# Kernel optimization log

Hardware: AMD Instinct MI355X
Metric: run time of the kernel (lower is better)

The kernel has to match this reference:

```python
import jax, jax.numpy as jnp
import numpy as np

N_NODES = 100000
N_REL = 6
E_PER_REL = 100000
HID = 256
EMB = 256
N_GRAPHS = 128
N_NODE_TYPES = 4
SUBTYPE_BUCKETS = 256


def setup_inputs() -> dict:
    key = jax.random.key(0)
    ks = jax.random.split(key, 20)
    s = 0.05
    return {
        "x_type": jax.random.randint(ks[0], (N_NODES,), 0, N_NODE_TYPES),
        "x_sub": jax.random.randint(ks[1], (N_NODES,), 0, SUBTYPE_BUCKETS),
        "edges": jax.random.randint(ks[2], (N_REL, 2, E_PER_REL), 0, N_NODES),
        "batch_ids": jnp.sort(jax.random.randint(ks[3], (N_NODES,), 0, N_GRAPHS)),
        "n_graphs": N_GRAPHS,
        "type_emb": jax.random.normal(ks[4], (N_NODE_TYPES, HID // 2), jnp.float32) * s,
        "sub_emb": jax.random.normal(ks[5], (SUBTYPE_BUCKETS, HID // 2), jnp.float32) * s,
        "W_rel0": jax.random.normal(ks[6], (N_REL, HID, HID), jnp.float32) * s,
        "W_self0": jax.random.normal(ks[7], (HID, HID), jnp.float32) * s,
        "b0": jnp.zeros((HID,), jnp.float32),
        "W_rel1": jax.random.normal(ks[8], (N_REL, HID, HID), jnp.float32) * s,
        "W_self1": jax.random.normal(ks[9], (HID, HID), jnp.float32) * s,
        "b1": jnp.zeros((HID,), jnp.float32),
        "pW1": jax.random.normal(ks[10], (HID, HID), jnp.float32) * s,
        "pb1": jnp.zeros((HID,), jnp.float32),
        "pW2": jax.random.normal(ks[11], (HID, EMB), jnp.float32) * s,
        "pb2": jnp.zeros((EMB,), jnp.float32),
    }


def _rgcn_layer(h, edges, W_rel, W_self, b, n):
    # edges: (R, 2, E); h: (N, H)
    src, tgt = edges[:, 0, :], edges[:, 1, :]  # (R, E)
    # per-relation gather -> matmul: (R, E, H) @ (R, H, D) -> (R, E, D)
    msg = jnp.einsum('reh,rhd->red', h[src], W_rel)
    tgt_flat = tgt.reshape(-1)
    out = jax.ops.segment_sum(msg.reshape(-1, msg.shape[-1]), tgt_flat, num_segments=n)
    total_deg = jax.ops.segment_sum(jnp.ones_like(tgt_flat, dtype=h.dtype), tgt_flat, num_segments=n)
    total_deg = jnp.clip(total_deg, 1.0)[:, None]
    out = out / total_deg + h @ W_self + b
    return jax.nn.relu(out)


def _mean_pool(h, batch_ids, n_graphs):
    summed = jax.ops.segment_sum(h, batch_ids, num_segments=n_graphs)
    count = jax.ops.segment_sum(jnp.ones((h.shape[0],), h.dtype), batch_ids, num_segments=n_graphs)
    return summed / jnp.clip(count, 1.0)[:, None]


def reference(x_type, x_sub, edges, batch_ids, n_graphs, type_emb, sub_emb,
              W_rel0, W_self0, b0, W_rel1, W_self1, b1, pW1, pb1, pW2, pb2):
    n = x_type.shape[0]
    h = jnp.concatenate([type_emb[x_type], sub_emb[x_sub]], axis=-1)  # (N, HID)
    h = _rgcn_layer(h, edges, W_rel0, W_self0, b0, n)
    h = _rgcn_layer(h, edges, W_rel1, W_self1, b1, n)
    pooled = _mean_pool(h, batch_ids, n_graphs)  # (G, HID)
    return jax.nn.relu(pooled @ pW1 + pb1) @ pW2 + pb2  # (G, EMB)
```

## Files before the change

### kernel.cpp

```cpp
#include <hip/hip_runtime.h>

#define NN    100000
#define NEDGE 100000
#define NRELS 6
#define HIDD  256
#define NGR   128
#define NKEY  (NRELS * NN)
#define NEDGT (NRELS * NEDGE)
#define WFRAG_ELEMS (4 * 7 * 16 * 2 * 64 * 8)
#define SMASK 0xFFFFF

typedef __bf16 bf16;
typedef __bf16 bf16x4 __attribute__((ext_vector_type(4)));
typedef __bf16 bf16x8 __attribute__((ext_vector_type(8)));
typedef float  f32x4  __attribute__((ext_vector_type(4)));
typedef float  f32x16 __attribute__((ext_vector_type(16)));

__device__ __forceinline__ float readlane_f(float v, int sl) {
    return __int_as_float(__builtin_amdgcn_readlane(__float_as_int(v), sl));
}

__global__ __launch_bounds__(256)
void hist_kernel(const int* __restrict__ edges, int* __restrict__ hist)
{
    int i = blockIdx.x * 256 + threadIdx.x;
    if (i >= NEDGT) return;
    int r = i / NEDGE;
    int e = i - r * NEDGE;
    int t = edges[r * (2 * NEDGE) + NEDGE + e];
    atomicAdd(&hist[r * NN + t], 1);
}

__global__ __launch_bounds__(256)
void scan_l0(const int* __restrict__ in, int* __restrict__ out, int* __restrict__ bsum, int n)
{
    __shared__ int sdata[256];
    const int t = threadIdx.x;
    const int base = blockIdx.x * 2048 + t * 8;
    int v[8]; int s = 0;
#pragma unroll
    for (int i = 0; i < 8; ++i) {
        int idx = base + i;
        int x = (idx < n) ? in[idx] : 0;
        v[i] = s; s += x;
    }
    sdata[t] = s;
    __syncthreads();
    for (int off = 1; off < 256; off <<= 1) {
        int y = (t >= off) ? sdata[t - off] : 0;
        __syncthreads();
        sdata[t] += y;
        __syncthreads();
    }
    int excl = sdata[t] - s;
#pragma unroll
    for (int i = 0; i < 8; ++i) {
        int idx = base + i;
        if (idx < n) out[idx] = excl + v[i];
    }
    if (t == 0) bsum[blockIdx.x] = sdata[255];
}

__global__ __launch_bounds__(256)
void scan_l1(int* __restrict__ bsum, int n)
{
    __shared__ int sdata[256];
    const int t = threadIdx.x;
    const int base = t * 8;
    int v[8]; int s = 0;
#pragma unroll
    for (int i = 0; i < 8; ++i) {
        int idx = base + i;
        int x = (idx < n) ? bsum[idx] : 0;
        v[i] = s; s += x;
    }
    sdata[t] = s;
    __syncthreads();
    for (int off = 1; off < 256; off <<= 1) {
        int y = (t >= off) ? sdata[t - off] : 0;
        __syncthreads();
        sdata[t] += y;
        __syncthreads();
    }
    int excl = sdata[t] - s;
#pragma unroll
    for (int i = 0; i < 8; ++i) {
        int idx = base + i;
        if (idx < n) bsum[idx] = excl + v[i];
    }
}

__global__ __launch_bounds__(256)
void scan_l2(int* __restrict__ offs, int* __restrict__ cursor, const int* __restrict__ bsum,
             const int* __restrict__ hist, float* __restrict__ invdeg,
             const int* __restrict__ batch_ids, float* __restrict__ cnt, int n)
{
    int idx = blockIdx.x * 256 + threadIdx.x;
    if (idx == 0) offs[NKEY] = NEDGT;

    {
        const int lane = threadIdx.x & 63;
        const bool valid = idx < NN;
        const int gv = valid ? batch_ids[idx] : -1;
        const int gprev = __shfl(gv, lane - 1);
        const bool head = valid && (lane == 0 || gv != gprev);
        const bool stop = head || !valid;
        const unsigned long long mask = __ballot(stop);
        if (head) {
            unsigned long long above = (lane == 63) ? 0ull : (mask >> (lane + 1));
            const int next = above ? (lane + 1 + __builtin_ctzll(above)) : 64;
            atomicAdd(&cnt[gv], (float)(next - lane));
        }
    }

    if (idx < NN) {
        int d = 0;
#pragma unroll
        for (int r = 0; r < NRELS; ++r) d += hist[r * NN + idx];
        invdeg[idx] = 1.0f / fmaxf((float)d, 1.0f);
    }
    if (idx >= n) return;
    int v = offs[idx] + bsum[idx >> 11];
    offs[idx] = v;
    cursor[idx] = v;
}

__global__ __launch_bounds__(256)
void scatter_kernel(const int* __restrict__ edges, int* __restrict__ cursor,
                    int* __restrict__ epack)
{
    int i = blockIdx.x * 256 + threadIdx.x;
    if (i >= NEDGT) return;
    int r = i / NEDGE;
    int e = i - r * NEDGE;
    int s = edges[r * (2 * NEDGE) + e];
    int t = edges[r * (2 * NEDGE) + NEDGE + e];
    int pos = atomicAdd(&cursor[r * NN + t], 1);
    epack[pos] = s | ((t & 15) << 20);
}

__global__ __launch_bounds__(256)
void build_wfrag(const float* __restrict__ Wr0, const float* __restrict__ Ws0,
                 const float* __restrict__ Wr1, const float* __restrict__ Ws1,
                 bf16* __restrict__ Wf0, bf16* __restrict__ Wf1)
{
    const int seg = blockIdx.x;
    const int step = blockIdx.y;
    const int layer = blockIdx.z;
    const int tid = threadIdx.x;
    const int w = tid >> 6;
    const int lane = tid & 63;
    const int l31 = lane & 31;
    const int lhi = lane >> 5;

    const float* Wr = layer ? Wr1 : Wr0;
    const float* Ws = layer ? Ws1 : Ws0;
    const float* src = (seg < 6) ? (Wr + ((size_t)seg << 16)) : Ws;
    bf16* Wf = layer ? Wf1 : Wf0;

    const int kb = step * 16 + lhi * 8;
#pragma unroll
    for (int ct = 0; ct < 2; ++ct) {
        const int n = w * 64 + ct * 32 + l31;
        bf16x8 o;
#pragma unroll
        for (int j = 0; j < 8; ++j)
            o[j] = (bf16)src[(size_t)(kb + j) * 256 + n];
        const size_t fb_idx = (size_t)(((w * 7 + seg) * 16 + step) * 2 + ct) * 64 + lane;
        *(bf16x8*)(Wf + fb_idx * 8) = o;
    }
}

template<bool L0, bool POOL>
__global__ __launch_bounds__(256, 3)
void rgcn_fused(const bf16* __restrict__ hin,
                const int* __restrict__ xt, const int* __restrict__ xs,
                const float* __restrict__ temb, const float* __restrict__ semb,
                const bf16* __restrict__ Wfrag, const float* __restrict__ bias,
                const float* __restrict__ invdeg, const int* __restrict__ offs,
                const int* __restrict__ epack, const int* __restrict__ batch_ids,
                float* __restrict__ pooled, bf16* __restrict__ hout)
{
    constexpr int DEPTH = L0 ? 8 : 16;
    const int m0 = blockIdx.x * 64;
    const int tid = threadIdx.x;
    const int lane = tid & 63;
    const int w = tid >> 6;
    const int l31 = lane & 31;
    const int lhi = lane >> 5;
    const int rbase = w * 16;

    __shared__ __align__(16) bf16 As[64 * HIDD];

    f32x16 acc[2][2] = {};

    int ivrow = m0 + rbase + (lane & 15);
    if (ivrow >= NN) ivrow = NN - 1;
    const float ivreg = invdeg[ivrow];

    for (int seg = 0; seg < 7; ++seg) {
        __syncthreads();

#pragma unroll
        for (int z = 0; z < 8; ++z) {
            const int row = rbase + lhi * 8 + z;
            const int unit = row * 32 + (l31 ^ (row & 7));
            *(bf16x8*)&As[unit * 8] = (bf16x8)(bf16)0.0f;
        }

        if (seg == 6) {
#pragma unroll
            for (int z = 0; z < 8; ++z) {
                const int row = rbase + lhi * 8 + z;
                const int gr = m0 + row;
                if (gr < NN) {
                    bf16x8 o;
                    if (L0) {
                        const int f0 = l31 * 8;
                        const float* src = (f0 < 128) ? (temb + xt[gr] * 128 + f0)
                                                      : (semb + xs[gr] * 128 + (f0 - 128));
                        f32x4 x0 = *(const f32x4*)src;
                        f32x4 x1 = *(const f32x4*)(src + 4);
                        o[0] = (bf16)x0[0]; o[1] = (bf16)x0[1];
                        o[2] = (bf16)x0[2]; o[3] = (bf16)x0[3];
                        o[4] = (bf16)x1[0]; o[5] = (bf16)x1[1];
                        o[6] = (bf16)x1[2]; o[7] = (bf16)x1[3];
                    } else {
                        o = *(const bf16x8*)(hin + ((size_t)gr << 8) + l31 * 8);
                    }
                    const int unit = row * 32 + (l31 ^ (row & 7));
                    *(bf16x8*)&As[unit * 8] = o;
                }
            }
        } else {
            const int gr0 = m0 + rbase;
            if (gr0 < NN) {
                const int rend = (gr0 + 16 < NN) ? (gr0 + 16) : NN;
                int st = offs[seg * NN + gr0];
                const int en = offs[seg * NN + rend];

                float a0 = 0.f, a1 = 0.f, a2 = 0.f, a3 = 0.f;
                int cur = -1;

                while (st < en) {
                    const int cnt = (en - st < 64) ? (en - st) : 64;
                    const int idx = st + ((lane < cnt) ? lane : (cnt - 1));
                    const int pv = epack[idx];
                    int at = 0, bt = 0;
                    if (L0) { const int sl = pv & SMASK; at = xt[sl]; bt = xs[sl]; }

                    for (int base = 0; base < cnt; base += DEPTH) {
                        f32x4  fb[L0 ? DEPTH : 1];
                        bf16x4 hb[L0 ? 1 : DEPTH];
#pragma unroll
                        for (int p = 0; p < DEPTH; ++p) {
                            int ip = base + p;
                            ip = (ip < cnt) ? ip : (cnt - 1);
                            if (L0) {
                                const int a = __builtin_amdgcn_readlane(at, ip);
                                const int b = __builtin_amdgcn_readlane(bt, ip);
                                const float* srcp = (lane < 32)
                                    ? temb + a * 128 + lane * 4
                                    : semb + b * 128 + (lane - 32) * 4;
                                fb[p] = *(const f32x4*)srcp;
                            } else {
                                const int s = __builtin_amdgcn_readlane(pv, ip) & SMASK;
                                hb[p] = *(const bf16x4*)(hin + ((size_t)s << 8) + lane * 4);
                            }
                        }
#pragma unroll
                        for (int p = 0; p < DEPTH; ++p) {
                            if (base + p < cnt) {
                                const int t = __builtin_amdgcn_readlane(pv, base + p) >> 20;
                                if (t != cur) {
                                    if (cur >= 0) {
                                        const float inv = readlane_f(ivreg, cur);
                                        bf16x4 o;
                                        o.x = (bf16)(a0 * inv); o.y = (bf16)(a1 * inv);
                                        o.z = (bf16)(a2 * inv); o.w = (bf16)(a3 * inv);
                                        const int row = rbase + cur;
                                        const int unit = row * 32 + ((lane >> 1) ^ (row & 7));
                                        *(bf16x4*)&As[unit * 8 + (lane & 1) * 4] = o;
                                    }
                                    cur = t; a0 = a1 = a2 = a3 = 0.f;
                                }
                                if (L0) {
                                    a0 += fb[p][0]; a1 += fb[p][1];
                                    a2 += fb[p][2]; a3 += fb[p][3];
                                } else {
                                    a0 += (float)hb[p].x; a1 += (float)hb[p].y;
                                    a2 += (float)hb[p].z; a3 += (float)hb[p].w;
                                }
                            }
                        }
                    }
                    st += cnt;
                }
                if (cur >= 0) {
                    const float inv = readlane_f(ivreg, cur);
                    bf16x4 o;
                    o.x = (bf16)(a0 * inv); o.y = (bf16)(a1 * inv);
                    o.z = (bf16)(a2 * inv); o.w = (bf16)(a3 * inv);
                    const int row = rbase + cur;
                    const int unit = row * 32 + ((lane >> 1) ^ (row & 7));
                    *(bf16x4*)&As[unit * 8 + (lane & 1) * 4] = o;
                }
            }
        }

        __syncthreads();

        const bf16* const wseg = Wfrag + ((size_t)((w * 7 + seg) * 16) * 2 * 64) * 8;
#pragma unroll
        for (int step = 0; step < 16; ++step) {
            bf16x8 b0 = *(const bf16x8*)(wseg + ((size_t)(step * 2 + 0) * 64 + lane) * 8);
            bf16x8 b1 = *(const bf16x8*)(wseg + ((size_t)(step * 2 + 1) * 64 + lane) * 8);
            const int ku = step * 2 + lhi;
            bf16x8 a0 = *(const bf16x8*)&As[(l31 * 32 + (ku ^ (l31 & 7))) * 8];
            bf16x8 a1 = *(const bf16x8*)&As[((32 + l31) * 32 + (ku ^ (l31 & 7))) * 8];
            acc[0][0] = __builtin_amdgcn_mfma_f32_32x32x16_bf16(a0, b0, acc[0][0], 0, 0, 0);
            acc[0][1] = __builtin_amdgcn_mfma_f32_32x32x16_bf16(a0, b1, acc[0][1], 0, 0, 0);
            acc[1][0] = __builtin_amdgcn_mfma_f32_32x32x16_bf16(a1, b0, acc[1][0], 0, 0, 0);
            acc[1][1] = __builtin_amdgcn_mfma_f32_32x32x16_bf16(a1, b1, acc[1][1], 0, 0, 0);
        }
    }

    float bcol[2];
#pragma unroll
    for (int ct = 0; ct < 2; ++ct) bcol[ct] = bias[w * 64 + ct * 32 + l31];

    if constexpr (POOL) {
        __syncthreads();
        int* bidArr = (int*)As;
        if (tid < 64) {
            const int r = m0 + tid;
            bidArr[tid] = (r < NN) ? batch_ids[r] : -1;
        }
        __syncthreads();
        const int last = (m0 + 63 < NN) ? 63 : (NN - 1 - m0);
        const int glo = bidArr[0];
        const int ghi = bidArr[last];
        for (int g = glo; g <= ghi; ++g) {
            float s0 = 0.f, s1 = 0.f;
#pragma unroll
            for (int rt = 0; rt < 2; ++rt) {
#pragma unroll
                for (int reg = 0; reg < 16; ++reg) {
                    const int rl = rt * 32 + (reg & 3) + 8 * (reg >> 2) + 4 * lhi;
                    if (bidArr[rl] == g) {
                        s0 += fmaxf(acc[rt][0][reg] + bcol[0], 0.0f);
                        s1 += fmaxf(acc[rt][1][reg] + bcol[1], 0.0f);
                    }
                }
            }
            s0 += __shfl_xor(s0, 32);
            s1 += __shfl_xor(s1, 32);
            if (lhi == 0) {
                atomicAdd(&pooled[g * HIDD + w * 64 + l31], s0);
                atomicAdd(&pooled[g * HIDD + w * 64 + 32 + l31], s1);
            }
        }
    } else {
#pragma unroll
        for (int rt = 0; rt < 2; ++rt) {
#pragma unroll
            for (int reg = 0; reg < 16; ++reg) {
                const int row = m0 + rt * 32 + (reg & 3) + 8 * (reg >> 2) + 4 * lhi;
                if (row < NN) {
#pragma unroll
                    for (int ct = 0; ct < 2; ++ct) {
                        const int col = w * 64 + ct * 32 + l31;
                        float v = acc[rt][ct][reg] + bcol[ct];
                        hout[((size_t)row << 8) + col] = (bf16)fmaxf(v, 0.0f);
                    }
                }
            }
        }
    }
}

__global__ __launch_bounds__(256)
void mlp_kernel(const float* __restrict__ pooled, const float* __restrict__ cnt,
                const float* __restrict__ pW1, const float* __restrict__ pb1,
                const float* __restrict__ pW2, const float* __restrict__ pb2,
                float* __restrict__ out)
{
    const int g = blockIdx.x;
    const int d = threadIdx.x;
    __shared__ float pn[HIDD];
    __shared__ float mid[HIDD];
    float c = fmaxf(cnt[g], 1.0f);
    pn[d] = pooled[g * HIDD + d] / c;
    __syncthreads();
    float s = pb1[d];
    for (int k = 0; k < HIDD; ++k) s = fmaf(pn[k], pW1[k * HIDD + d], s);
    mid[d] = fmaxf(s, 0.0f);
    __syncthreads();
    float s2 = pb2[d];
    for (int k = 0; k < HIDD; ++k) s2 = fmaf(mid[k], pW2[k * HIDD + d], s2);
    out[g * HIDD + d] = s2;
}

extern "C" void kernel_launch(void* const* d_in, const int* in_sizes, int n_in,
                              void* d_out, int out_size, void* d_ws, size_t ws_size,
                              hipStream_t stream)
{
    const int*   x_type    = (const int*)d_in[0];
    const int*   x_sub     = (const int*)d_in[1];
    const int*   edges     = (const int*)d_in[2];
    const int*   batch_ids = (const int*)d_in[3];
    const float* type_emb  = (const float*)d_in[5];
    const float* sub_emb   = (const float*)d_in[6];
    const float* W_rel0    = (const float*)d_in[7];
    const float* W_self0   = (const float*)d_in[8];
    const float* b0        = (const float*)d_in[9];
    const float* W_rel1    = (const float*)d_in[10];
    const float* W_self1   = (const float*)d_in[11];
    const float* b1        = (const float*)d_in[12];
    const float* pW1       = (const float*)d_in[13];
    const float* pb1       = (const float*)d_in[14];
    const float* pW2       = (const float*)d_in[15];
    const float* pb2       = (const float*)d_in[16];
    float* out = (float*)d_out;

    char* p = (char*)d_ws;
    auto carve = [&](size_t bytes) { char* q = p; p += (bytes + 255) & ~255ull; return q; };
    bf16*  h1     = (bf16*) carve((size_t)NN * HIDD * sizeof(bf16));
    bf16*  Wf0    = (bf16*) carve((size_t)WFRAG_ELEMS * sizeof(bf16));
    bf16*  Wf1    = (bf16*) carve((size_t)WFRAG_ELEMS * sizeof(bf16));
    float* invdeg = (float*)carve((size_t)NN * sizeof(float));
    int*   hist   = (int*)  carve((size_t)NKEY * sizeof(int));
    int*   offs   = (int*)  carve((size_t)(NKEY + 1) * sizeof(int));
    int*   cursor = (int*)  carve((size_t)NKEY * sizeof(int));
    int*   bsum   = (int*)  carve(2048 * sizeof(int));
    int*   epack  = (int*)  carve((size_t)NEDGT * sizeof(int));
    float* pooled = (float*)carve((size_t)NGR * HIDD * sizeof(float));
    float* cnt    = (float*)carve((size_t)NGR * sizeof(float));

    hipMemsetAsync(hist, 0, (size_t)NKEY * sizeof(int), stream);
    hipMemsetAsync(pooled, 0, (size_t)(NGR * HIDD + NGR) * sizeof(float), stream);

    const int NB0 = (NKEY + 2047) / 2048;
    hist_kernel<<<(NEDGT + 255) / 256, 256, 0, stream>>>(edges, hist);
    scan_l0<<<NB0, 256, 0, stream>>>(hist, offs, bsum, NKEY);
    scan_l1<<<1, 256, 0, stream>>>(bsum, NB0);
    scan_l2<<<(NKEY + 255) / 256, 256, 0, stream>>>(offs, cursor, bsum, hist, invdeg,
                                                    batch_ids, cnt, NKEY);
    scatter_kernel<<<(NEDGT + 255) / 256, 256, 0, stream>>>(edges, cursor, epack);

    dim3 wgrid(7, 16, 2);
    build_wfrag<<<wgrid, 256, 0, stream>>>(W_rel0, W_self0, W_rel1, W_self1, Wf0, Wf1);

    const int FGRID = (NN + 63) / 64;
    rgcn_fused<true, false><<<FGRID, 256, 0, stream>>>(
        nullptr, x_type, x_sub, type_emb, sub_emb,
        Wf0, b0, invdeg, offs, epack, batch_ids, pooled, h1);
    rgcn_fused<false, true><<<FGRID, 256, 0, stream>>>(
        h1, x_type, x_sub, type_emb, sub_emb,
        Wf1, b1, invdeg, offs, epack, batch_ids, pooled, nullptr);

    mlp_kernel<<<NGR, 256, 0, stream>>>(pooled, cnt, pW1, pb1, pW2, pb2, out);
}
```

Before: 540.5 us.

## Precombine embedding table in bf16 and shard pooled atomics

Builds a 1024x256 bf16 table holding every combination of type and subtype embedding. The scatter stage now stores each edge's combined embedding index, so layer 0's gather uses the same bf16 path as layer 1 with depth 16, replacing two indirect index loads and fp32 gathers. Pooled sums are also spread across 8 shards by block index to reduce atomic contention, and the MLP kernel adds the shards back together. This costs an extra edge array, a table-building kernel, a larger memset, and rounding the layer-0 inputs to bf16.

Result: no change. 543.5 us (+0.6%).

```diff
diff --git a/kernel.cpp b/kernel.cpp
--- a/kernel.cpp
+++ b/kernel.cpp
@@ -9,6 +9,7 @@
 #define NEDGT (NRELS * NEDGE)
 #define WFRAG_ELEMS (4 * 7 * 16 * 2 * 64 * 8)
 #define SMASK 0xFFFFF
+#define NSHARD 8
 
 typedef __bf16 bf16;
 typedef __bf16 bf16x4 __attribute__((ext_vector_type(4)));
@@ -127,7 +128,8 @@
 
 __global__ __launch_bounds__(256)
 void scatter_kernel(const int* __restrict__ edges, int* __restrict__ cursor,
-                    int* __restrict__ epack)
+                    const int* __restrict__ xt, const int* __restrict__ xs,
+                    int* __restrict__ epack, int* __restrict__ epack2)
 {
     int i = blockIdx.x * 256 + threadIdx.x;
     if (i >= NEDGT) return;
@@ -137,6 +139,18 @@
     int t = edges[r * (2 * NEDGE) + NEDGE + e];
     int pos = atomicAdd(&cursor[r * NN + t], 1);
     epack[pos] = s | ((t & 15) << 20);
+    epack2[pos] = xt[s] * 256 + xs[s];
+}
+
+__global__ __launch_bounds__(256)
+void build_etab(const float* __restrict__ temb, const float* __restrict__ semb,
+                bf16* __restrict__ etab)
+{
+    const int c = blockIdx.x;
+    const int f = threadIdx.x;
+    const int t = c >> 8, s = c & 255;
+    float v = (f < 128) ? temb[t * 128 + f] : semb[s * 128 + (f - 128)];
+    etab[c * 256 + f] = (bf16)v;
 }
 
 __global__ __launch_bounds__(256)
@@ -178,10 +192,11 @@
                 const float* __restrict__ temb, const float* __restrict__ semb,
                 const bf16* __restrict__ Wfrag, const float* __restrict__ bias,
                 const float* __restrict__ invdeg, const int* __restrict__ offs,
-                const int* __restrict__ epack, const int* __restrict__ batch_ids,
+                const int* __restrict__ epack, const int* __restrict__ epack2,
+                const int* __restrict__ batch_ids,
                 float* __restrict__ pooled, bf16* __restrict__ hout)
 {
-    constexpr int DEPTH = L0 ? 8 : 16;
+    constexpr int DEPTH = 16;
     const int m0 = blockIdx.x * 64;
     const int tid = threadIdx.x;
     const int lane = tid & 63;
@@ -246,27 +261,17 @@
                     const int cnt = (en - st < 64) ? (en - st) : 64;
                     const int idx = st + ((lane < cnt) ? lane : (cnt - 1));
                     const int pv = epack[idx];
-                    int at = 0, bt = 0;
-                    if (L0) { const int sl = pv & SMASK; at = xt[sl]; bt = xs[sl]; }
+                    const int rv = L0 ? epack2[idx]
+                                      : (pv & SMASK);
 
                     for (int base = 0; base < cnt; base += DEPTH) {
-                        f32x4  fb[L0 ? DEPTH : 1];
-                        bf16x4 hb[L0 ? 1 : DEPTH];
+                        bf16x4 hb[DEPTH];
 #pragma unroll
                         for (int p = 0; p < DEPTH; ++p) {
                             int ip = base + p;
                             ip = (ip < cnt) ? ip : (cnt - 1);
-                            if (L0) {
-                                const int a = __builtin_amdgcn_readlane(at, ip);
-                                const int b = __builtin_amdgcn_readlane(bt, ip);
-                                const float* srcp = (lane < 32)
-                                    ? temb + a * 128 + lane * 4
-                                    : semb + b * 128 + (lane - 32) * 4;
-                                fb[p] = *(const f32x4*)srcp;
-                            } else {
-                                const int s = __builtin_amdgcn_readlane(pv, ip) & SMASK;
-                                hb[p] = *(const bf16x4*)(hin + ((size_t)s << 8) + lane * 4);
-                            }
+                            const int s = __builtin_amdgcn_readlane(rv, ip);
+                            hb[p] = *(const bf16x4*)(hin + ((size_t)s << 8) + lane * 4);
                         }
 #pragma unroll
                         for (int p = 0; p < DEPTH; ++p) {
@@ -284,13 +289,8 @@
                                     }
                                     cur = t; a0 = a1 = a2 = a3 = 0.f;
                                 }
-                                if (L0) {
-                                    a0 += fb[p][0]; a1 += fb[p][1];
-                                    a2 += fb[p][2]; a3 += fb[p][3];
-                                } else {
-                                    a0 += (float)hb[p].x; a1 += (float)hb[p].y;
-                                    a2 += (float)hb[p].z; a3 += (float)hb[p].w;
-                                }
+                                a0 += (float)hb[p].x; a1 += (float)hb[p].y;
+                                a2 += (float)hb[p].z; a3 += (float)hb[p].w;
                             }
                         }
                     }
@@ -330,6 +330,7 @@
     for (int ct = 0; ct < 2; ++ct) bcol[ct] = bias[w * 64 + ct * 32 + l31];
 
     if constexpr (POOL) {
+        float* pshard = pooled + (size_t)(blockIdx.x & (NSHARD - 1)) * NGR * HIDD;
         __syncthreads();
         int* bidArr = (int*)As;
         if (tid < 64) {
@@ -356,8 +357,8 @@
             s0 += __shfl_xor(s0, 32);
             s1 += __shfl_xor(s1, 32);
             if (lhi == 0) {
-                atomicAdd(&pooled[g * HIDD + w * 64 + l31], s0);
-                atomicAdd(&pooled[g * HIDD + w * 64 + 32 + l31], s1);
+                atomicAdd(&pshard[g * HIDD + w * 64 + l31], s0);
+                atomicAdd(&pshard[g * HIDD + w * 64 + 32 + l31], s1);
             }
         }
     } else {
@@ -390,7 +391,11 @@
     __shared__ float pn[HIDD];
     __shared__ float mid[HIDD];
     float c = fmaxf(cnt[g], 1.0f);
-    pn[d] = pooled[g * HIDD + d] / c;
+    float sacc = 0.f;
+#pragma unroll
+    for (int x = 0; x < NSHARD; ++x)
+        sacc += pooled[(size_t)x * NGR * HIDD + g * HIDD + d];
+    pn[d] = sacc / c;
     __syncthreads();
     float s = pb1[d];
     for (int k = 0; k < HIDD; ++k) s = fmaf(pn[k], pW1[k * HIDD + d], s);
@@ -428,17 +433,19 @@
     bf16*  h1     = (bf16*) carve((size_t)NN * HIDD * sizeof(bf16));
     bf16*  Wf0    = (bf16*) carve((size_t)WFRAG_ELEMS * sizeof(bf16));
     bf16*  Wf1    = (bf16*) carve((size_t)WFRAG_ELEMS * sizeof(bf16));
+    bf16*  etab   = (bf16*) carve((size_t)1024 * 256 * sizeof(bf16));
     float* invdeg = (float*)carve((size_t)NN * sizeof(float));
     int*   hist   = (int*)  carve((size_t)NKEY * sizeof(int));
     int*   offs   = (int*)  carve((size_t)(NKEY + 1) * sizeof(int));
     int*   cursor = (int*)  carve((size_t)NKEY * sizeof(int));
     int*   bsum   = (int*)  carve(2048 * sizeof(int));
     int*   epack  = (int*)  carve((size_t)NEDGT * sizeof(int));
-    float* pooled = (float*)carve((size_t)NGR * HIDD * sizeof(float));
+    int*   epack2 = (int*)  carve((size_t)NEDGT * sizeof(int));
+    float* pooled = (float*)carve((size_t)NSHARD * NGR * HIDD * sizeof(float));
     float* cnt    = (float*)carve((size_t)NGR * sizeof(float));
 
     hipMemsetAsync(hist, 0, (size_t)NKEY * sizeof(int), stream);
-    hipMemsetAsync(pooled, 0, (size_t)(NGR * HIDD + NGR) * sizeof(float), stream);
+    hipMemsetAsync(pooled, 0, (size_t)(NSHARD * NGR * HIDD + NGR) * sizeof(float), stream);
 
     const int NB0 = (NKEY + 2047) / 2048;
     hist_kernel<<<(NEDGT + 255) / 256, 256, 0, stream>>>(edges, hist);
@@ -446,18 +453,20 @@
     scan_l1<<<1, 256, 0, stream>>>(bsum, NB0);
     scan_l2<<<(NKEY + 255) / 256, 256, 0, stream>>>(offs, cursor, bsum, hist, invdeg,
                                                     batch_ids, cnt, NKEY);
-    scatter_kernel<<<(NEDGT + 255) / 256, 256, 0, stream>>>(edges, cursor, epack);
+    scatter_kernel<<<(NEDGT + 255) / 256, 256, 0, stream>>>(edges, cursor, x_type, x_sub,
+                                                            epack, epack2);
+    build_etab<<<1024, 256, 0, stream>>>(type_emb, sub_emb, etab);
 
     dim3 wgrid(7, 16, 2);
     build_wfrag<<<wgrid, 256, 0, stream>>>(W_rel0, W_self0, W_rel1, W_self1, Wf0, Wf1);
 
     const int FGRID = (NN + 63) / 64;
     rgcn_fused<true, false><<<FGRID, 256, 0, stream>>>(
-        nullptr, x_type, x_sub, type_emb, sub_emb,
-        Wf0, b0, invdeg, offs, epack, batch_ids, pooled, h1);
+        etab, x_type, x_sub, type_emb, sub_emb,
+        Wf0, b0, invdeg, offs, epack, epack2, batch_ids, pooled, h1);
     rgcn_fused<false, true><<<FGRID, 256, 0, stream>>>(
         h1, x_type, x_sub, type_emb, sub_emb,
-        Wf1, b1, invdeg, offs, epack, batch_ids, pooled, nullptr);
+        Wf1, b1, invdeg, offs, epack, epack2, batch_ids, pooled, nullptr);
 
     mlp_kernel<<<NGR, 256, 0, stream>>>(pooled, cnt, pW1, pb1, pW2, pb2, out);
 }
```
